# Performance work log

Measured on AMD Instinct MI355X. Metric: run time of the kernel, lower is better.

Reference implementation:

```python
import jax, jax.numpy as jnp
import numpy as np
import math

B, L, D = 2, 2048, 1024
H = 16
DH = D // H


def setup_inputs() -> dict:
    key = jax.random.key(0)
    k1, k2, k3, k4 = jax.random.split(key, 4)
    s = 1.0 / math.sqrt(D)
    return {
        "x": jax.random.normal(k1, (B, L, D), dtype=jnp.float32),
        "w_in": jax.random.normal(k2, (3 * D, D), dtype=jnp.float32) * s,
        "b_in": jax.random.normal(k3, (3 * D,), dtype=jnp.float32) * 0.01,
        "w_out": jax.random.normal(k4, (D, D), dtype=jnp.float32) * s,
        "causal_mask": 1,
    }


def reference(x, w_in, b_in, w_out, causal_mask):
    b, seq_len, d = x.shape
    # fused QKV projection: (B,L,3D)
    qkv = x @ w_in.T + b_in
    q, k, v = jnp.split(qkv, 3, axis=-1)
    # (B,L,D) -> (B,H,L,DH)
    def heads(t):
        return t.reshape(b, seq_len, H, DH).transpose(0, 2, 1, 3)
    q, k, v = heads(q), heads(k), heads(v)
    scores = jnp.einsum("bhqd,bhkd->bhqk", q, k) / math.sqrt(DH)
    if causal_mask:
        causal = jnp.triu(jnp.ones((seq_len, seq_len), dtype=bool), k=1)
        scores = jnp.where(causal[None, None, :, :], jnp.float32(-1e9), scores)
    # stable softmax (amax-subtract as in original)
    weight = jax.nn.softmax(scores, axis=-1)
    out = jnp.einsum("bhqk,bhkd->bhqd", weight, v)
    out = out.transpose(0, 2, 1, 3).reshape(b, seq_len, d)
    return out @ w_out.T
```

## Files before the change

### kernel.cpp

```cpp
#include <hip/hip_runtime.h>
#include <hip/hip_bf16.h>

typedef __attribute__((ext_vector_type(8))) short short8;
typedef __attribute__((ext_vector_type(4))) short short4v;
typedef __attribute__((ext_vector_type(4))) float f32x4;

#define BB 2
#define LL 2048
#define DD 1024
#define HH 16
#define DHH 64
#define KK 1024

__device__ __forceinline__ void gload_lds16(const void* g, void* l) {
  __builtin_amdgcn_global_load_lds((const __attribute__((address_space(1))) void*)g,
                                   (__attribute__((address_space(3))) void*)l,
                                   16, 0, 0);
}

__device__ __forceinline__ f32x4 splat4(float x) {
  f32x4 v; v[0] = x; v[1] = x; v[2] = x; v[3] = x; return v;
}

__device__ __forceinline__ unsigned short f2b(float x) {
  __hip_bfloat16 h = __float2bfloat16(x);
  return *reinterpret_cast<unsigned short*>(&h);
}

#define NX8  ((BB * LL * DD) / 8)
#define NWI8 ((3 * DD * DD) / 8)
#define NWO8 ((DD * DD) / 8)
__global__ void cvt_all(const float* __restrict__ x,
                        const float* __restrict__ w_in,
                        const float* __restrict__ w_out,
                        __hip_bfloat16* __restrict__ xb,
                        __hip_bfloat16* __restrict__ w_inb,
                        __hip_bfloat16* __restrict__ w_outb) {
  int i = blockIdx.x * blockDim.x + threadIdx.x;
  const float* src;
  __hip_bfloat16* dst;
  int j;
  if (i < NX8)              { src = x;     dst = xb;     j = i; }
  else if (i < NX8 + NWI8)  { src = w_in;  dst = w_inb;  j = i - NX8; }
  else                      { src = w_out; dst = w_outb; j = i - NX8 - NWI8; }
  const f32x4 a = ((const f32x4*)src)[j * 2];
  const f32x4 b = ((const f32x4*)src)[j * 2 + 1];
  short8 o;
#pragma unroll
  for (int k = 0; k < 4; ++k) o[k] = (short)f2b(a[k]);
#pragma unroll
  for (int k = 0; k < 4; ++k) o[4 + k] = (short)f2b(b[k]);
  ((short8*)dst)[j] = o;
}

template<bool QKV>
__global__ void gemm_bt(const __hip_bfloat16* __restrict__ A,
                        const __hip_bfloat16* __restrict__ Bm,
                        const float* __restrict__ bias,
                        __hip_bfloat16* __restrict__ Cq,
                        __hip_bfloat16* __restrict__ Ck,
                        __hip_bfloat16* __restrict__ Cv,
                        float* __restrict__ Cd,
                        int N, int nbn) {
  __shared__ __align__(16) char As[8192];
  __shared__ __align__(16) char Bs[8192];
  const int tid = threadIdx.x;
  const int lane = tid & 63, wid = tid >> 6;
  const int l15 = lane & 15, lhi = lane >> 4;
  const int wm = wid >> 1, wn = wid & 1;
  const int bn = blockIdx.x % nbn, bm = blockIdx.x / nbn;
  const int m0 = bm * 128, n0 = bn * 128;

  f32x4 acc[4][4] = {};

  for (int kt = 0; kt < KK / 32; ++kt) {
    const int k0 = kt * 32;
    __syncthreads();
#pragma unroll
    for (int j = 0; j < 2; ++j) {
      int c = wid * 128 + j * 64 + lane;
      int row = c >> 2;
      int ab = ((c & 3) * 16) ^ (((row >> 1) & 3) << 4);
      gload_lds16(A + (size_t)(m0 + row) * KK + k0 + (ab >> 1),
                  As + wid * 2048 + j * 1024);
    }
#pragma unroll
    for (int j = 0; j < 2; ++j) {
      int c = wid * 128 + j * 64 + lane;
      int row = c >> 2;
      int ab = ((c & 3) * 16) ^ (((row >> 1) & 3) << 4);
      gload_lds16(Bm + (size_t)(n0 + row) * KK + k0 + (ab >> 1),
                  Bs + wid * 2048 + j * 1024);
    }
    __syncthreads();

    short8 af[4], bf[4];
#pragma unroll
    for (int mf = 0; mf < 4; ++mf) {
      int row = wm * 64 + mf * 16 + l15;
      int byt = (lhi * 16) ^ (((row >> 1) & 3) << 4);
      af[mf] = *(const short8*)(As + row * 64 + byt);
    }
#pragma unroll
    for (int nf = 0; nf < 4; ++nf) {
      int row = wn * 64 + nf * 16 + l15;
      int byt = (lhi * 16) ^ (((row >> 1) & 3) << 4);
      bf[nf] = *(const short8*)(Bs + row * 64 + byt);
    }
#pragma unroll
    for (int mf = 0; mf < 4; ++mf)
#pragma unroll
      for (int nf = 0; nf < 4; ++nf)
        acc[mf][nf] = __builtin_amdgcn_mfma_f32_16x16x32_bf16(af[mf], bf[nf],
                                                              acc[mf][nf], 0, 0, 0);
  }

#pragma unroll
  for (int mf = 0; mf < 4; ++mf) {
#pragma unroll
    for (int nf = 0; nf < 4; ++nf) {
      const int n = n0 + wn * 64 + nf * 16 + l15;
      if constexpr (QKV) {
        const int sect = n >> 10;
        const int nn = n & 1023;
        const int h = nn >> 6, dh = nn & 63;
        const float bv = bias[n];
        const int m_base = m0 + wm * 64 + mf * 16 + lhi * 4;
        const int b = m_base >> 11, ml = m_base & 2047;
        if (sect == 2) {
          short4v v;
#pragma unroll
          for (int r = 0; r < 4; ++r) v[r] = (short)f2b(acc[mf][nf][r] + bv);
          *(short4v*)&Cv[(((size_t)(b * HH + h)) * DHH + dh) * LL + ml] = v;
        } else {
          __hip_bfloat16* dst = (sect == 0) ? Cq : Ck;
#pragma unroll
          for (int r = 0; r < 4; ++r)
            dst[(((size_t)(b * HH + h)) * LL + ml + r) * DHH + dh] =
                __float2bfloat16(acc[mf][nf][r] + bv);
        }
      } else {
#pragma unroll
        for (int r = 0; r < 4; ++r) {
          const int m = m0 + wm * 64 + mf * 16 + lhi * 4 + r;
          Cd[(size_t)m * N + n] = acc[mf][nf][r];
        }
      }
    }
  }
}

__global__ __launch_bounds__(128) void attn_fwd(
    const __hip_bfloat16* __restrict__ Q,
    const __hip_bfloat16* __restrict__ K,
    const __hip_bfloat16* __restrict__ VT,
    __hip_bfloat16* __restrict__ att,
    const int* __restrict__ maskp) {
  __shared__ __align__(16) char Pbuf[2][4096];
  __shared__ __align__(16) float Ob[32][68];
  __shared__ float Mb[32], Lb[32];
  const int tid = threadIdx.x;
  const int lane = tid & 63, wid = tid >> 6;
  const int l15 = lane & 15, lhi = lane >> 4;
  const int bid = blockIdx.x;
  const int strip = 63 - (bid >> 5);
  const int bh = bid & 31;
  const int causal = *maskp;
  const int r0 = strip * 32;
  const __hip_bfloat16* Qg = Q + (size_t)bh * LL * DHH;
  const __hip_bfloat16* Kg = K + (size_t)bh * LL * DHH;
  const __hip_bfloat16* VTg = VT + (size_t)bh * DHH * LL;
  char* Pw = Pbuf[wid];

  short8 aq[2][2];
#pragma unroll
  for (int mf = 0; mf < 2; ++mf)
#pragma unroll
    for (int ks = 0; ks < 2; ++ks)
      aq[mf][ks] = *(const short8*)(Qg + (size_t)(r0 + mf * 16 + l15) * DHH +
                                    ks * 32 + lhi * 8);

  f32x4 o[2][4] = {};
  f32x4 mrun[2], lrun[2];
  mrun[0] = splat4(-1e30f); mrun[1] = splat4(-1e30f);
  lrun[0] = splat4(0.0f);   lrun[1] = splat4(0.0f);

  const int nt = causal ? ((r0 + 31) >> 6) + 1 : (LL / 64);
  const int hf = (nt + 1) >> 1;
  const int t0 = wid ? hf : 0;
  const int t1 = wid ? nt : hf;

  for (int t = t0; t < t1; ++t) {
    const int kv0 = t * 64;
    short8 bk[4][2];
#pragma unroll
    for (int nf = 0; nf < 4; ++nf)
#pragma unroll
      for (int ks = 0; ks < 2; ++ks)
        bk[nf][ks] = *(const short8*)(Kg + (size_t)(kv0 + nf * 16 + l15) * DHH +
                                      ks * 32 + lhi * 8);
    short8 bv[4][2];
#pragma unroll
    for (int nf = 0; nf < 4; ++nf)
#pragma unroll
      for (int ks = 0; ks < 2; ++ks)
        bv[nf][ks] = *(const short8*)(VTg + (size_t)(nf * 16 + l15) * LL +
                                      kv0 + ks * 32 + lhi * 8);

    f32x4 s[2][4] = {};
    __builtin_amdgcn_s_setprio(1);
#pragma unroll
    for (int mf = 0; mf < 2; ++mf)
#pragma unroll
      for (int nf = 0; nf < 4; ++nf) {
        s[mf][nf] = __builtin_amdgcn_mfma_f32_16x16x32_bf16(aq[mf][0], bk[nf][0], s[mf][nf], 0, 0, 0);
        s[mf][nf] = __builtin_amdgcn_mfma_f32_16x16x32_bf16(aq[mf][1], bk[nf][1], s[mf][nf], 0, 0, 0);
      }
    __builtin_amdgcn_s_setprio(0);

    const bool needmask = causal && (kv0 + 63 > r0);
#pragma unroll
    for (int mf = 0; mf < 2; ++mf)
#pragma unroll
      for (int nf = 0; nf < 4; ++nf) {
        const int kv = kv0 + nf * 16 + l15;
#pragma unroll
        for (int r = 0; r < 4; ++r) {
          float v = s[mf][nf][r] * 0.125f;
          if (needmask && kv > r0 + mf * 16 + lhi * 4 + r) v = -1e30f;
          s[mf][nf][r] = v;
        }
      }
#pragma unroll
    for (int mf = 0; mf < 2; ++mf) {
      f32x4 pm = s[mf][0];
#pragma unroll
      for (int nf = 1; nf < 4; ++nf)
#pragma unroll
        for (int r = 0; r < 4; ++r) pm[r] = fmaxf(pm[r], s[mf][nf][r]);
#pragma unroll
      for (int d = 1; d < 16; d <<= 1)
#pragma unroll
        for (int r = 0; r < 4; ++r) pm[r] = fmaxf(pm[r], __shfl_xor(pm[r], d, 64));

      f32x4 mnew, rsum;
#pragma unroll
      for (int r = 0; r < 4; ++r) {
        mnew[r] = fmaxf(mrun[mf][r], pm[r]);
        float sc = __expf(mrun[mf][r] - mnew[r]);
        lrun[mf][r] *= sc;
        rsum[r] = 0.0f;
#pragma unroll
        for (int nf = 0; nf < 4; ++nf) o[mf][nf][r] *= sc;
      }
#pragma unroll
      for (int nf = 0; nf < 4; ++nf)
#pragma unroll
        for (int r = 0; r < 4; ++r) {
          float p = __expf(s[mf][nf][r] - mnew[r]);
          s[mf][nf][r] = p;
          rsum[r] += p;
        }
#pragma unroll
      for (int d = 1; d < 16; d <<= 1)
#pragma unroll
        for (int r = 0; r < 4; ++r) rsum[r] += __shfl_xor(rsum[r], d, 64);
#pragma unroll
      for (int r = 0; r < 4; ++r) lrun[mf][r] += rsum[r];
      mrun[mf] = mnew;
    }
#pragma unroll
    for (int mf = 0; mf < 2; ++mf)
#pragma unroll
      for (int nf = 0; nf < 4; ++nf)
#pragma unroll
        for (int r = 0; r < 4; ++r) {
          const int row = mf * 16 + lhi * 4 + r;
          const int cb = (nf * 16 + l15) * 2;
          *(__hip_bfloat16*)(Pw + row * 128 + (cb ^ ((row & 12) << 3))) =
              __float2bfloat16(s[mf][nf][r]);
        }
    short8 ap[2][2];
#pragma unroll
    for (int mf = 0; mf < 2; ++mf)
#pragma unroll
      for (int ks = 0; ks < 2; ++ks) {
        const int row = mf * 16 + l15;
        const int cb = ks * 64 + lhi * 16;
        ap[mf][ks] = *(const short8*)(Pw + row * 128 + (cb ^ ((row & 12) << 3)));
      }
    __builtin_amdgcn_s_setprio(1);
#pragma unroll
    for (int mf = 0; mf < 2; ++mf)
#pragma unroll
      for (int nf = 0; nf < 4; ++nf) {
        o[mf][nf] = __builtin_amdgcn_mfma_f32_16x16x32_bf16(ap[mf][0], bv[nf][0], o[mf][nf], 0, 0, 0);
        o[mf][nf] = __builtin_amdgcn_mfma_f32_16x16x32_bf16(ap[mf][1], bv[nf][1], o[mf][nf], 0, 0, 0);
      }
    __builtin_amdgcn_s_setprio(0);
  }

  __syncthreads();
  if (wid == 1) {
#pragma unroll
    for (int mf = 0; mf < 2; ++mf)
#pragma unroll
      for (int r = 0; r < 4; ++r) {
        const int row = mf * 16 + lhi * 4 + r;
        if (l15 == 0) { Mb[row] = mrun[mf][r]; Lb[row] = lrun[mf][r]; }
#pragma unroll
        for (int nf = 0; nf < 4; ++nf)
          Ob[row][nf * 16 + l15] = o[mf][nf][r];
      }
  }
  __syncthreads();
  if (wid == 0) {
    const int b = bh >> 4, h = bh & 15;
#pragma unroll
    for (int mf = 0; mf < 2; ++mf)
#pragma unroll
      for (int r = 0; r < 4; ++r) {
        const int row = mf * 16 + lhi * 4 + r;
        const float m1 = Mb[row], l1 = Lb[row];
        const float m0 = mrun[mf][r], l0 = lrun[mf][r];
        const float mt = fmaxf(m0, m1);
        const float sc0 = __expf(m0 - mt), sc1 = __expf(m1 - mt);
        const float inv = 1.0f / (l0 * sc0 + l1 * sc1);
        const int grow = r0 + row;
#pragma unroll
        for (int nf = 0; nf < 4; ++nf)
          att[((size_t)(b * LL + grow)) * DD + h * DHH + nf * 16 + l15] =
              __float2bfloat16((o[mf][nf][r] * sc0 + Ob[row][nf * 16 + l15] * sc1) * inv);
      }
  }
}

extern "C" void kernel_launch(void* const* d_in, const int* in_sizes, int n_in,
                              void* d_out, int out_size, void* d_ws, size_t ws_size,
                              hipStream_t stream) {
  const float* x     = (const float*)d_in[0];
  const float* w_in  = (const float*)d_in[1];
  const float* b_in  = (const float*)d_in[2];
  const float* w_out = (const float*)d_in[3];
  const int* mask    = (const int*)d_in[4];
  float* out = (float*)d_out;

  char* ws = (char*)d_ws;
  const size_t MiB = 1024u * 1024u;
  __hip_bfloat16* xb    = (__hip_bfloat16*)(ws);
  __hip_bfloat16* w_inb = (__hip_bfloat16*)(ws + 8 * MiB);
  __hip_bfloat16* w_outb= (__hip_bfloat16*)(ws + 14 * MiB);
  __hip_bfloat16* Qb    = (__hip_bfloat16*)(ws + 16 * MiB);
  __hip_bfloat16* Kb    = (__hip_bfloat16*)(ws + 24 * MiB);
  __hip_bfloat16* Vtb   = (__hip_bfloat16*)(ws + 32 * MiB);
  __hip_bfloat16* att   = (__hip_bfloat16*)(ws + 40 * MiB);

  cvt_all<<<dim3(4096), dim3(256), 0, stream>>>(x, w_in, w_out, xb, w_inb, w_outb);

  gemm_bt<true><<<dim3(32 * 24), dim3(256), 0, stream>>>(
      xb, w_inb, b_in, Qb, Kb, Vtb, nullptr, 3072, 24);
  attn_fwd<<<dim3(2048), dim3(128), 0, stream>>>(Qb, Kb, Vtb, att, mask);
  gemm_bt<false><<<dim3(32 * 8), dim3(256), 0, stream>>>(
      att, w_outb, nullptr, nullptr, nullptr, nullptr, out, 1024, 8);
}
```

Before: 139.5 us.

## Pair causal strips per block, split KV across four waves, use exp2

The attention kernel now runs 1024 blocks of 256 threads. Each block handles two query strips, one long and one short, so causal work per block is balanced. The KV tiles of each strip are split across four waves, and the partial results are merged through LDS with a two-step reduction tree. The softmax now uses native exp2 with the log2(e) factor folded into the scale constant. In exchange there are more __syncthreads barriers and more LDS use per block, and the short-strip phase leaves some waves with very few tiles.

```diff
diff --git a/kernel.cpp b/kernel.cpp
--- a/kernel.cpp
+++ b/kernel.cpp
@@ -11,6 +11,8 @@
 #define HH 16
 #define DHH 64
 #define KK 1024
+#define SCL 0.18033688011112042f
+#define EXP2(x) __builtin_amdgcn_exp2f(x)
 
 __device__ __forceinline__ void gload_lds16(const void* g, void* l) {
   __builtin_amdgcn_global_load_lds((const __attribute__((address_space(1))) void*)g,
@@ -150,188 +152,212 @@
   }
 }
 
-__global__ __launch_bounds__(128) void attn_fwd(
+__global__ __launch_bounds__(256, 4) void attn_fwd(
     const __hip_bfloat16* __restrict__ Q,
     const __hip_bfloat16* __restrict__ K,
     const __hip_bfloat16* __restrict__ VT,
     __hip_bfloat16* __restrict__ att,
     const int* __restrict__ maskp) {
-  __shared__ __align__(16) char Pbuf[2][4096];
-  __shared__ __align__(16) float Ob[32][68];
-  __shared__ float Mb[32], Lb[32];
+  __shared__ __align__(16) char Pbuf[4][4096];
+  __shared__ __align__(16) float Ob[2][32][68];
+  __shared__ float Mb[2][32], Lb[2][32];
   const int tid = threadIdx.x;
   const int lane = tid & 63, wid = tid >> 6;
   const int l15 = lane & 15, lhi = lane >> 4;
   const int bid = blockIdx.x;
-  const int strip = 63 - (bid >> 5);
+  const int pair = bid >> 5;
   const int bh = bid & 31;
   const int causal = *maskp;
-  const int r0 = strip * 32;
   const __hip_bfloat16* Qg = Q + (size_t)bh * LL * DHH;
   const __hip_bfloat16* Kg = K + (size_t)bh * LL * DHH;
   const __hip_bfloat16* VTg = VT + (size_t)bh * DHH * LL;
   char* Pw = Pbuf[wid];
-
-  short8 aq[2][2];
-#pragma unroll
-  for (int mf = 0; mf < 2; ++mf)
-#pragma unroll
-    for (int ks = 0; ks < 2; ++ks)
-      aq[mf][ks] = *(const short8*)(Qg + (size_t)(r0 + mf * 16 + l15) * DHH +
-                                    ks * 32 + lhi * 8);
-
-  f32x4 o[2][4] = {};
-  f32x4 mrun[2], lrun[2];
-  mrun[0] = splat4(-1e30f); mrun[1] = splat4(-1e30f);
-  lrun[0] = splat4(0.0f);   lrun[1] = splat4(0.0f);
-
-  const int nt = causal ? ((r0 + 31) >> 6) + 1 : (LL / 64);
-  const int hf = (nt + 1) >> 1;
-  const int t0 = wid ? hf : 0;
-  const int t1 = wid ? nt : hf;
-
-  for (int t = t0; t < t1; ++t) {
-    const int kv0 = t * 64;
-    short8 bk[4][2];
-#pragma unroll
-    for (int nf = 0; nf < 4; ++nf)
+  const int b_ = bh >> 4, h = bh & 15;
+
+  for (int ph = 0; ph < 2; ++ph) {
+    const int strip = ph ? pair : (63 - pair);
+    const int r0 = strip * 32;
+
+    short8 aq[2][2];
+#pragma unroll
+    for (int mf = 0; mf < 2; ++mf)
 #pragma unroll
       for (int ks = 0; ks < 2; ++ks)
-        bk[nf][ks] = *(const short8*)(Kg + (size_t)(kv0 + nf * 16 + l15) * DHH +
+        aq[mf][ks] = *(const short8*)(Qg + (size_t)(r0 + mf * 16 + l15) * DHH +
                                       ks * 32 + lhi * 8);
-    short8 bv[4][2];
-#pragma unroll
-    for (int nf = 0; nf < 4; ++nf)
-#pragma unroll
-      for (int ks = 0; ks < 2; ++ks)
-        bv[nf][ks] = *(const short8*)(VTg + (size_t)(nf * 16 + l15) * LL +
-                                      kv0 + ks * 32 + lhi * 8);
-
-    f32x4 s[2][4] = {};
-    __builtin_amdgcn_s_setprio(1);
-#pragma unroll
-    for (int mf = 0; mf < 2; ++mf)
-#pragma unroll
-      for (int nf = 0; nf < 4; ++nf) {
-        s[mf][nf] = __builtin_amdgcn_mfma_f32_16x16x32_bf16(aq[mf][0], bk[nf][0], s[mf][nf], 0, 0, 0);
-        s[mf][nf] = __builtin_amdgcn_mfma_f32_16x16x32_bf16(aq[mf][1], bk[nf][1], s[mf][nf], 0, 0, 0);
+
+    f32x4 o[2][4] = {};
+    f32x4 mrun[2], lrun[2];
+    mrun[0] = splat4(-1e30f); mrun[1] = splat4(-1e30f);
+    lrun[0] = splat4(0.0f);   lrun[1] = splat4(0.0f);
+
+    const int nt = causal ? ((r0 + 31) >> 6) + 1 : (LL / 64);
+    const int t0 = (wid * nt) >> 2;
+    const int t1 = ((wid + 1) * nt) >> 2;
+
+    for (int t = t0; t < t1; ++t) {
+      const int kv0 = t * 64;
+      short8 bk[4][2];
+#pragma unroll
+      for (int nf = 0; nf < 4; ++nf)
+#pragma unroll
+        for (int ks = 0; ks < 2; ++ks)
+          bk[nf][ks] = *(const short8*)(Kg + (size_t)(kv0 + nf * 16 + l15) * DHH +
+                                        ks * 32 + lhi * 8);
+      short8 bv[4][2];
+#pragma unroll
+      for (int nf = 0; nf < 4; ++nf)
+#pragma unroll
+        for (int ks = 0; ks < 2; ++ks)
+          bv[nf][ks] = *(const short8*)(VTg + (size_t)(nf * 16 + l15) * LL +
+                                        kv0 + ks * 32 + lhi * 8);
+
+      f32x4 s[2][4] = {};
+      __builtin_amdgcn_s_setprio(1);
+#pragma unroll
+      for (int mf = 0; mf < 2; ++mf)
+#pragma unroll
+        for (int nf = 0; nf < 4; ++nf) {
+          s[mf][nf] = __builtin_amdgcn_mfma_f32_16x16x32_bf16(aq[mf][0], bk[nf][0], s[mf][nf], 0, 0, 0);
+          s[mf][nf] = __builtin_amdgcn_mfma_f32_16x16x32_bf16(aq[mf][1], bk[nf][1], s[mf][nf], 0, 0, 0);
+        }
+      __builtin_amdgcn_s_setprio(0);
+
+      const bool needmask = causal && (kv0 + 63 > r0);
+#pragma unroll
+      for (int mf = 0; mf < 2; ++mf)
+#pragma unroll
+        for (int nf = 0; nf < 4; ++nf) {
+          const int kv = kv0 + nf * 16 + l15;
+#pragma unroll
+          for (int r = 0; r < 4; ++r) {
+            float v = s[mf][nf][r] * SCL;
+            if (needmask && kv > r0 + mf * 16 + lhi * 4 + r) v = -1e30f;
+            s[mf][nf][r] = v;
+          }
+        }
+#pragma unroll
+      for (int mf = 0; mf < 2; ++mf) {
+        f32x4 pm = s[mf][0];
+#pragma unroll
+        for (int nf = 1; nf < 4; ++nf)
+#pragma unroll
+          for (int r = 0; r < 4; ++r) pm[r] = fmaxf(pm[r], s[mf][nf][r]);
+#pragma unroll
+        for (int d = 1; d < 16; d <<= 1)
+#pragma unroll
+          for (int r = 0; r < 4; ++r) pm[r] = fmaxf(pm[r], __shfl_xor(pm[r], d, 64));
+
+        f32x4 mnew, rsum;
+#pragma unroll
+        for (int r = 0; r < 4; ++r) {
+          mnew[r] = fmaxf(mrun[mf][r], pm[r]);
+          float sc = EXP2(mrun[mf][r] - mnew[r]);
+          lrun[mf][r] *= sc;
+          rsum[r] = 0.0f;
+#pragma unroll
+          for (int nf = 0; nf < 4; ++nf) o[mf][nf][r] *= sc;
+        }
+#pragma unroll
+        for (int nf = 0; nf < 4; ++nf)
+#pragma unroll
+          for (int r = 0; r < 4; ++r) {
+            float p = EXP2(s[mf][nf][r] - mnew[r]);
+            s[mf][nf][r] = p;
+            rsum[r] += p;
+          }
+#pragma unroll
+        for (int d = 1; d < 16; d <<= 1)
+#pragma unroll
+          for (int r = 0; r < 4; ++r) rsum[r] += __shfl_xor(rsum[r], d, 64);
+#pragma unroll
+        for (int r = 0; r < 4; ++r) lrun[mf][r] += rsum[r];
+        mrun[mf] = mnew;
       }
-    __builtin_amdgcn_s_setprio(0);
-
-    const bool needmask = causal && (kv0 + 63 > r0);
-#pragma unroll
-    for (int mf = 0; mf < 2; ++mf)
-#pragma unroll
-      for (int nf = 0; nf < 4; ++nf) {
-        const int kv = kv0 + nf * 16 + l15;
-#pragma unroll
-        for (int r = 0; r < 4; ++r) {
-          float v = s[mf][nf][r] * 0.125f;
-          if (needmask && kv > r0 + mf * 16 + lhi * 4 + r) v = -1e30f;
-          s[mf][nf][r] = v;
-        }
-      }
-#pragma unroll
-    for (int mf = 0; mf < 2; ++mf) {
-      f32x4 pm = s[mf][0];
-#pragma unroll
-      for (int nf = 1; nf < 4; ++nf)
-#pragma unroll
-        for (int r = 0; r < 4; ++r) pm[r] = fmaxf(pm[r], s[mf][nf][r]);
-#pragma unroll
-      for (int d = 1; d < 16; d <<= 1)
-#pragma unroll
-        for (int r = 0; r < 4; ++r) pm[r] = fmaxf(pm[r], __shfl_xor(pm[r], d, 64));
-
-      f32x4 mnew, rsum;
-#pragma unroll
-      for (int r = 0; r < 4; ++r) {
-        mnew[r] = fmaxf(mrun[mf][r], pm[r]);
-        float sc = __expf(mrun[mf][r] - mnew[r]);
-        lrun[mf][r] *= sc;
-        rsum[r] = 0.0f;
-#pragma unroll
-        for (int nf = 0; nf < 4; ++nf) o[mf][nf][r] *= sc;
-      }
-#pragma unroll
-      for (int nf = 0; nf < 4; ++nf)
-#pragma unroll
-        for (int r = 0; r < 4; ++r) {
-          float p = __expf(s[mf][nf][r] - mnew[r]);
-          s[mf][nf][r] = p;
-          rsum[r] += p;
-        }
-#pragma unroll
-      for (int d = 1; d < 16; d <<= 1)
-#pragma unroll
-        for (int r = 0; r < 4; ++r) rsum[r] += __shfl_xor(rsum[r], d, 64);
-#pragma unroll
-      for (int r = 0; r < 4; ++r) lrun[mf][r] += rsum[r];
-      mrun[mf] = mnew;
-    }
-#pragma unroll
-    for (int mf = 0; mf < 2; ++mf)
-#pragma unroll
-      for (int nf = 0; nf < 4; ++nf)
+#pragma unroll
+      for (int mf = 0; mf < 2; ++mf)
+#pragma unroll
+        for (int nf = 0; nf < 4; ++nf)
+#pragma unroll
+          for (int r = 0; r < 4; ++r) {
+            const int row = mf * 16 + lhi * 4 + r;
+            const int cb = (nf * 16 + l15) * 2;
+            *(__hip_bfloat16*)(Pw + row * 128 + (cb ^ ((row & 12) << 3))) =
+                __float2bfloat16(s[mf][nf][r]);
+          }
+      short8 ap[2][2];
+#pragma unroll
+      for (int mf = 0; mf < 2; ++mf)
+#pragma unroll
+        for (int ks = 0; ks < 2; ++ks) {
+          const int row = mf * 16 + l15;
+          const int cb = ks * 64 + lhi * 16;
+          ap[mf][ks] = *(const short8*)(Pw + row * 128 + (cb ^ ((row & 12) << 3)));
+        }
+      __builtin_amdgcn_s_setprio(1);
+#pragma unroll
+      for (int mf = 0; mf < 2; ++mf)
+#pragma unroll
+        for (int nf = 0; nf < 4; ++nf) {
+          o[mf][nf] = __builtin_amdgcn_mfma_f32_16x16x32_bf16(ap[mf][0], bv[nf][0], o[mf][nf], 0, 0, 0);
+          o[mf][nf] = __builtin_amdgcn_mfma_f32_16x16x32_bf16(ap[mf][1], bv[nf][1], o[mf][nf], 0, 0, 0);
+        }
+      __builtin_amdgcn_s_setprio(0);
+    }
+
+    auto dump = [&](int b) {
+#pragma unroll
+      for (int mf = 0; mf < 2; ++mf)
 #pragma unroll
         for (int r = 0; r < 4; ++r) {
           const int row = mf * 16 + lhi * 4 + r;
-          const int cb = (nf * 16 + l15) * 2;
-          *(__hip_bfloat16*)(Pw + row * 128 + (cb ^ ((row & 12) << 3))) =
-              __float2bfloat16(s[mf][nf][r]);
-        }
-    short8 ap[2][2];
-#pragma unroll
-    for (int mf = 0; mf < 2; ++mf)
-#pragma unroll
-      for (int ks = 0; ks < 2; ++ks) {
-        const int row = mf * 16 + l15;
-        const int cb = ks * 64 + lhi * 16;
-        ap[mf][ks] = *(const short8*)(Pw + row * 128 + (cb ^ ((row & 12) << 3)));
-      }
-    __builtin_amdgcn_s_setprio(1);
-#pragma unroll
-    for (int mf = 0; mf < 2; ++mf)
-#pragma unroll
-      for (int nf = 0; nf < 4; ++nf) {
-        o[mf][nf] = __builtin_amdgcn_mfma_f32_16x16x32_bf16(ap[mf][0], bv[nf][0], o[mf][nf], 0, 0, 0);
-        o[mf][nf] = __builtin_amdgcn_mfma_f32_16x16x32_bf16(ap[mf][1], bv[nf][1], o[mf][nf], 0, 0, 0);
-      }
-    __builtin_amdgcn_s_setprio(0);
-  }
-
-  __syncthreads();
-  if (wid == 1) {
-#pragma unroll
-    for (int mf = 0; mf < 2; ++mf)
-#pragma unroll
-      for (int r = 0; r < 4; ++r) {
-        const int row = mf * 16 + lhi * 4 + r;
-        if (l15 == 0) { Mb[row] = mrun[mf][r]; Lb[row] = lrun[mf][r]; }
-#pragma unroll
-        for (int nf = 0; nf < 4; ++nf)
-          Ob[row][nf * 16 + l15] = o[mf][nf][r];
-      }
-  }
-  __syncthreads();
-  if (wid == 0) {
-    const int b = bh >> 4, h = bh & 15;
-#pragma unroll
-    for (int mf = 0; mf < 2; ++mf)
-#pragma unroll
-      for (int r = 0; r < 4; ++r) {
-        const int row = mf * 16 + lhi * 4 + r;
-        const float m1 = Mb[row], l1 = Lb[row];
-        const float m0 = mrun[mf][r], l0 = lrun[mf][r];
-        const float mt = fmaxf(m0, m1);
-        const float sc0 = __expf(m0 - mt), sc1 = __expf(m1 - mt);
-        const float inv = 1.0f / (l0 * sc0 + l1 * sc1);
-        const int grow = r0 + row;
-#pragma unroll
-        for (int nf = 0; nf < 4; ++nf)
-          att[((size_t)(b * LL + grow)) * DD + h * DHH + nf * 16 + l15] =
-              __float2bfloat16((o[mf][nf][r] * sc0 + Ob[row][nf * 16 + l15] * sc1) * inv);
-      }
+          if (l15 == 0) { Mb[b][row] = mrun[mf][r]; Lb[b][row] = lrun[mf][r]; }
+#pragma unroll
+          for (int nf = 0; nf < 4; ++nf)
+            Ob[b][row][nf * 16 + l15] = o[mf][nf][r];
+        }
+    };
+    auto combine = [&](int b) {
+#pragma unroll
+      for (int mf = 0; mf < 2; ++mf)
+#pragma unroll
+        for (int r = 0; r < 4; ++r) {
+          const int row = mf * 16 + lhi * 4 + r;
+          const float mo = Mb[b][row], lo = Lb[b][row];
+          const float mt = fmaxf(mrun[mf][r], mo);
+          const float sr = EXP2(mrun[mf][r] - mt);
+          const float so = EXP2(mo - mt);
+          lrun[mf][r] = lrun[mf][r] * sr + lo * so;
+          mrun[mf][r] = mt;
+#pragma unroll
+          for (int nf = 0; nf < 4; ++nf)
+            o[mf][nf][r] = o[mf][nf][r] * sr + Ob[b][row][nf * 16 + l15] * so;
+        }
+    };
+
+    __syncthreads();
+    if (wid & 1) dump(wid >> 1);
+    __syncthreads();
+    if (!(wid & 1)) combine(wid >> 1);
+    __syncthreads();
+    if (wid == 2) dump(0);
+    __syncthreads();
+    if (wid == 0) {
+      combine(0);
+#pragma unroll
+      for (int mf = 0; mf < 2; ++mf)
+#pragma unroll
+        for (int r = 0; r < 4; ++r) {
+          const int row = mf * 16 + lhi * 4 + r;
+          const float inv = 1.0f / lrun[mf][r];
+          const int grow = r0 + row;
+#pragma unroll
+          for (int nf = 0; nf < 4; ++nf)
+            att[((size_t)(b_ * LL + grow)) * DD + h * DHH + nf * 16 + l15] =
+                __float2bfloat16(o[mf][nf][r] * inv);
+        }
+    }
+    __syncthreads();
   }
 }
 
@@ -359,7 +385,7 @@
 
   gemm_bt<true><<<dim3(32 * 24), dim3(256), 0, stream>>>(
       xb, w_inb, b_in, Qb, Kb, Vtb, nullptr, 3072, 24);
-  attn_fwd<<<dim3(2048), dim3(128), 0, stream>>>(Qb, Kb, Vtb, att, mask);
+  attn_fwd<<<dim3(1024), dim3(256), 0, stream>>>(Qb, Kb, Vtb, att, mask);
   gemm_bt<false><<<dim3(32 * 8), dim3(256), 0, stream>>>(
       att, w_outb, nullptr, nullptr, nullptr, nullptr, out, 1024, 8);
 }
```

After: 237.8 us. +70.4%, slower.

## Transpose attention MFMAs, use exp2 softmax with lazy rescale and packed P stores

Applied to the files above, without the earlier changes.

Swaps the MFMA operand order so each lane owns one query row. Row max and sum then need only two cross-lane shuffles instead of four per register. Softmax now uses exp2 with log2e folded into the scale, and rescales the running max only when the new max exceeds the old by more than 8, which skips the o rescale on most tiles. P is written to LDS as packed 8-byte stores into a larger swizzled buffer, and the final merge uses vector stores. The risks are reduced precision from the lazy rescaling threshold, and removing launch_bounds may change register allocation.

```diff
diff --git a/kernel.cpp b/kernel.cpp
--- a/kernel.cpp
+++ b/kernel.cpp
@@ -11,15 +11,13 @@
 #define HH 16
 #define DHH 64
 #define KK 1024
+#define SCL 0.18033688011112042f
+#define EXP2(x) __builtin_amdgcn_exp2f(x)
 
 __device__ __forceinline__ void gload_lds16(const void* g, void* l) {
   __builtin_amdgcn_global_load_lds((const __attribute__((address_space(1))) void*)g,
                                    (__attribute__((address_space(3))) void*)l,
                                    16, 0, 0);
-}
-
-__device__ __forceinline__ f32x4 splat4(float x) {
-  f32x4 v; v[0] = x; v[1] = x; v[2] = x; v[3] = x; return v;
 }
 
 __device__ __forceinline__ unsigned short f2b(float x) {
@@ -150,13 +148,13 @@
   }
 }
 
-__global__ __launch_bounds__(128) void attn_fwd(
+__global__ void attn_fwd(
     const __hip_bfloat16* __restrict__ Q,
     const __hip_bfloat16* __restrict__ K,
     const __hip_bfloat16* __restrict__ VT,
     __hip_bfloat16* __restrict__ att,
     const int* __restrict__ maskp) {
-  __shared__ __align__(16) char Pbuf[2][4096];
+  __shared__ __align__(16) char Pbuf[2][8192];
   __shared__ __align__(16) float Ob[32][68];
   __shared__ float Mb[32], Lb[32];
   const int tid = threadIdx.x;
@@ -171,6 +169,7 @@
   const __hip_bfloat16* Kg = K + (size_t)bh * LL * DHH;
   const __hip_bfloat16* VTg = VT + (size_t)bh * DHH * LL;
   char* Pw = Pbuf[wid];
+  const int swz = l15 << 4;
 
   short8 aq[2][2];
 #pragma unroll
@@ -181,9 +180,8 @@
                                     ks * 32 + lhi * 8);
 
   f32x4 o[2][4] = {};
-  f32x4 mrun[2], lrun[2];
-  mrun[0] = splat4(-1e30f); mrun[1] = splat4(-1e30f);
-  lrun[0] = splat4(0.0f);   lrun[1] = splat4(0.0f);
+  float mrun[2] = {-1e30f, -1e30f};
+  float lrun[2] = {0.0f, 0.0f};
 
   const int nt = causal ? ((r0 + 31) >> 6) + 1 : (LL / 64);
   const int hf = (nt + 1) >> 1;
@@ -192,12 +190,12 @@
 
   for (int t = t0; t < t1; ++t) {
     const int kv0 = t * 64;
-    short8 bk[4][2];
+    short8 ka[4][2];
 #pragma unroll
     for (int nf = 0; nf < 4; ++nf)
 #pragma unroll
       for (int ks = 0; ks < 2; ++ks)
-        bk[nf][ks] = *(const short8*)(Kg + (size_t)(kv0 + nf * 16 + l15) * DHH +
+        ka[nf][ks] = *(const short8*)(Kg + (size_t)(kv0 + nf * 16 + l15) * DHH +
                                       ks * 32 + lhi * 8);
     short8 bv[4][2];
 #pragma unroll
@@ -210,128 +208,116 @@
     f32x4 s[2][4] = {};
     __builtin_amdgcn_s_setprio(1);
 #pragma unroll
-    for (int mf = 0; mf < 2; ++mf)
-#pragma unroll
-      for (int nf = 0; nf < 4; ++nf) {
-        s[mf][nf] = __builtin_amdgcn_mfma_f32_16x16x32_bf16(aq[mf][0], bk[nf][0], s[mf][nf], 0, 0, 0);
-        s[mf][nf] = __builtin_amdgcn_mfma_f32_16x16x32_bf16(aq[mf][1], bk[nf][1], s[mf][nf], 0, 0, 0);
+    for (int ks = 0; ks < 2; ++ks)
+#pragma unroll
+      for (int nf = 0; nf < 4; ++nf) {
+        s[0][nf] = __builtin_amdgcn_mfma_f32_16x16x32_bf16(ka[nf][ks], aq[0][ks], s[0][nf], 0, 0, 0);
+        s[1][nf] = __builtin_amdgcn_mfma_f32_16x16x32_bf16(ka[nf][ks], aq[1][ks], s[1][nf], 0, 0, 0);
       }
     __builtin_amdgcn_s_setprio(0);
 
     const bool needmask = causal && (kv0 + 63 > r0);
 #pragma unroll
-    for (int mf = 0; mf < 2; ++mf)
-#pragma unroll
-      for (int nf = 0; nf < 4; ++nf) {
-        const int kv = kv0 + nf * 16 + l15;
+    for (int mf = 0; mf < 2; ++mf) {
+      const int q = r0 + mf * 16 + l15;
+#pragma unroll
+      for (int nf = 0; nf < 4; ++nf) {
+        const int kvb = kv0 + nf * 16 + lhi * 4;
 #pragma unroll
         for (int r = 0; r < 4; ++r) {
-          float v = s[mf][nf][r] * 0.125f;
-          if (needmask && kv > r0 + mf * 16 + lhi * 4 + r) v = -1e30f;
+          float v = s[mf][nf][r] * SCL;
+          if (needmask && kvb + r > q) v = -1e30f;
           s[mf][nf][r] = v;
         }
       }
+      f32x4 t4 = s[mf][0];
+#pragma unroll
+      for (int nf = 1; nf < 4; ++nf)
+#pragma unroll
+        for (int r = 0; r < 4; ++r) t4[r] = fmaxf(t4[r], s[mf][nf][r]);
+      float pm = fmaxf(fmaxf(t4[0], t4[1]), fmaxf(t4[2], t4[3]));
+      pm = fmaxf(pm, __shfl_xor(pm, 16, 64));
+      pm = fmaxf(pm, __shfl_xor(pm, 32, 64));
+      if (__any(pm > mrun[mf] + 8.0f)) {
+        const float mnew = fmaxf(mrun[mf], pm);
+        const float sc = EXP2(mrun[mf] - mnew);
+        mrun[mf] = mnew;
+        lrun[mf] *= sc;
+#pragma unroll
+        for (int nf = 0; nf < 4; ++nf)
+#pragma unroll
+          for (int r = 0; r < 4; ++r) o[mf][nf][r] *= sc;
+      }
+      float rs = 0.0f;
+#pragma unroll
+      for (int nf = 0; nf < 4; ++nf)
+#pragma unroll
+        for (int r = 0; r < 4; ++r) {
+          float p = EXP2(s[mf][nf][r] - mrun[mf]);
+          s[mf][nf][r] = p;
+          rs += p;
+        }
+      rs += __shfl_xor(rs, 16, 64);
+      rs += __shfl_xor(rs, 32, 64);
+      lrun[mf] += rs;
+
+      char* base = Pw + (mf * 16 + l15) * 256;
+#pragma unroll
+      for (int nf = 0; nf < 4; ++nf) {
+        unsigned lo = (unsigned)f2b(s[mf][nf][0]) | ((unsigned)f2b(s[mf][nf][1]) << 16);
+        unsigned hi = (unsigned)f2b(s[mf][nf][2]) | ((unsigned)f2b(s[mf][nf][3]) << 16);
+        *(unsigned long long*)(base + ((nf * 32 + lhi * 8) ^ swz)) =
+            (unsigned long long)lo | ((unsigned long long)hi << 32);
+      }
+    }
+
+    __builtin_amdgcn_s_setprio(1);
 #pragma unroll
     for (int mf = 0; mf < 2; ++mf) {
-      f32x4 pm = s[mf][0];
-#pragma unroll
-      for (int nf = 1; nf < 4; ++nf)
-#pragma unroll
-        for (int r = 0; r < 4; ++r) pm[r] = fmaxf(pm[r], s[mf][nf][r]);
-#pragma unroll
-      for (int d = 1; d < 16; d <<= 1)
-#pragma unroll
-        for (int r = 0; r < 4; ++r) pm[r] = fmaxf(pm[r], __shfl_xor(pm[r], d, 64));
-
-      f32x4 mnew, rsum;
-#pragma unroll
-      for (int r = 0; r < 4; ++r) {
-        mnew[r] = fmaxf(mrun[mf][r], pm[r]);
-        float sc = __expf(mrun[mf][r] - mnew[r]);
-        lrun[mf][r] *= sc;
-        rsum[r] = 0.0f;
-#pragma unroll
-        for (int nf = 0; nf < 4; ++nf) o[mf][nf][r] *= sc;
-      }
+      const char* base = Pw + (mf * 16 + l15) * 256;
+      short8 ap0 = *(const short8*)(base + ((lhi * 16) ^ swz));
+      short8 ap1 = *(const short8*)(base + ((64 + lhi * 16) ^ swz));
+#pragma unroll
+      for (int nf = 0; nf < 4; ++nf) {
+        o[mf][nf] = __builtin_amdgcn_mfma_f32_16x16x32_bf16(bv[nf][0], ap0, o[mf][nf], 0, 0, 0);
+        o[mf][nf] = __builtin_amdgcn_mfma_f32_16x16x32_bf16(bv[nf][1], ap1, o[mf][nf], 0, 0, 0);
+      }
+    }
+    __builtin_amdgcn_s_setprio(0);
+  }
+
+  if (wid == 1) {
+#pragma unroll
+    for (int mf = 0; mf < 2; ++mf) {
+      const int row = mf * 16 + l15;
+      if (lhi == 0) { Mb[row] = mrun[mf]; Lb[row] = lrun[mf]; }
 #pragma unroll
       for (int nf = 0; nf < 4; ++nf)
-#pragma unroll
-        for (int r = 0; r < 4; ++r) {
-          float p = __expf(s[mf][nf][r] - mnew[r]);
-          s[mf][nf][r] = p;
-          rsum[r] += p;
-        }
-#pragma unroll
-      for (int d = 1; d < 16; d <<= 1)
-#pragma unroll
-        for (int r = 0; r < 4; ++r) rsum[r] += __shfl_xor(rsum[r], d, 64);
-#pragma unroll
-      for (int r = 0; r < 4; ++r) lrun[mf][r] += rsum[r];
-      mrun[mf] = mnew;
-    }
-#pragma unroll
-    for (int mf = 0; mf < 2; ++mf)
-#pragma unroll
-      for (int nf = 0; nf < 4; ++nf)
-#pragma unroll
-        for (int r = 0; r < 4; ++r) {
-          const int row = mf * 16 + lhi * 4 + r;
-          const int cb = (nf * 16 + l15) * 2;
-          *(__hip_bfloat16*)(Pw + row * 128 + (cb ^ ((row & 12) << 3))) =
-              __float2bfloat16(s[mf][nf][r]);
-        }
-    short8 ap[2][2];
-#pragma unroll
-    for (int mf = 0; mf < 2; ++mf)
-#pragma unroll
-      for (int ks = 0; ks < 2; ++ks) {
-        const int row = mf * 16 + l15;
-        const int cb = ks * 64 + lhi * 16;
-        ap[mf][ks] = *(const short8*)(Pw + row * 128 + (cb ^ ((row & 12) << 3)));
-      }
-    __builtin_amdgcn_s_setprio(1);
-#pragma unroll
-    for (int mf = 0; mf < 2; ++mf)
-#pragma unroll
-      for (int nf = 0; nf < 4; ++nf) {
-        o[mf][nf] = __builtin_amdgcn_mfma_f32_16x16x32_bf16(ap[mf][0], bv[nf][0], o[mf][nf], 0, 0, 0);
-        o[mf][nf] = __builtin_amdgcn_mfma_f32_16x16x32_bf16(ap[mf][1], bv[nf][1], o[mf][nf], 0, 0, 0);
-      }
-    __builtin_amdgcn_s_setprio(0);
-  }
-
-  __syncthreads();
-  if (wid == 1) {
-#pragma unroll
-    for (int mf = 0; mf < 2; ++mf)
-#pragma unroll
-      for (int r = 0; r < 4; ++r) {
-        const int row = mf * 16 + lhi * 4 + r;
-        if (l15 == 0) { Mb[row] = mrun[mf][r]; Lb[row] = lrun[mf][r]; }
-#pragma unroll
-        for (int nf = 0; nf < 4; ++nf)
-          Ob[row][nf * 16 + l15] = o[mf][nf][r];
-      }
+        *(f32x4*)&Ob[row][nf * 16 + lhi * 4] = o[mf][nf];
+    }
   }
   __syncthreads();
   if (wid == 0) {
-    const int b = bh >> 4, h = bh & 15;
-#pragma unroll
-    for (int mf = 0; mf < 2; ++mf)
-#pragma unroll
-      for (int r = 0; r < 4; ++r) {
-        const int row = mf * 16 + lhi * 4 + r;
-        const float m1 = Mb[row], l1 = Lb[row];
-        const float m0 = mrun[mf][r], l0 = lrun[mf][r];
-        const float mt = fmaxf(m0, m1);
-        const float sc0 = __expf(m0 - mt), sc1 = __expf(m1 - mt);
-        const float inv = 1.0f / (l0 * sc0 + l1 * sc1);
-        const int grow = r0 + row;
-#pragma unroll
-        for (int nf = 0; nf < 4; ++nf)
-          att[((size_t)(b * LL + grow)) * DD + h * DHH + nf * 16 + l15] =
-              __float2bfloat16((o[mf][nf][r] * sc0 + Ob[row][nf * 16 + l15] * sc1) * inv);
-      }
+    const int b_ = bh >> 4, h = bh & 15;
+#pragma unroll
+    for (int mf = 0; mf < 2; ++mf) {
+      const int row = mf * 16 + l15;
+      const float m1 = Mb[row], l1 = Lb[row];
+      const float mt = fmaxf(mrun[mf], m1);
+      const float sc0 = EXP2(mrun[mf] - mt);
+      const float sc1 = EXP2(m1 - mt);
+      const float inv = 1.0f / (lrun[mf] * sc0 + l1 * sc1);
+      __hip_bfloat16* dst = att + ((size_t)(b_ * LL + r0 + row)) * DD + h * DHH;
+#pragma unroll
+      for (int nf = 0; nf < 4; ++nf) {
+        f32x4 ov = *(const f32x4*)&Ob[row][nf * 16 + lhi * 4];
+        short4v pk;
+#pragma unroll
+        for (int r = 0; r < 4; ++r)
+          pk[r] = (short)f2b((o[mf][nf][r] * sc0 + ov[r] * sc1) * inv);
+        *(short4v*)(dst + nf * 16 + lhi * 4) = pk;
+      }
+    }
   }
 }
 
```

Result: slower. 209.6 us (+50.2%).
